# Optimization experiments

Hardware: AMD Instinct MI355X
Metric: run time of the kernel (lower is better)

Reference implementation:

```python
import jax, jax.numpy as jnp
import numpy as np

ATTRACTION_W = 1.0
REPULSION_W = 1.0
MARGIN = 0.3  # hardcoded local `margin = 0.3` in the torch forward


def setup_inputs() -> dict:
    key = jax.random.key(0)
    k1, k2, k3 = jax.random.split(key, 3)
    B, N, D, K = 16, 65536, 32, 512
    beta = jax.random.normal(k1, (B, N, 1), dtype=jnp.float32)
    embed = jax.random.normal(k2, (B, N, D), dtype=jnp.float32)
    # instance id per hit: -1 = background, 0..K-1 = instances
    sid = jax.random.randint(k3, (B, N), -1, K).astype(jnp.int32)
    # first K hits are the condensation points, one per instance
    sid = sid.at[:, :K].set(jnp.arange(K, dtype=jnp.int32)[None, :])
    is_cp = jnp.zeros((B, N), dtype=jnp.int32).at[:, :K].set(1)
    return {"beta": beta, "embed": embed, "slice_id": sid, "is_cp": is_cp, "num_instances": K}


def _per_batch(beta_b, emb_b, sid, iscp, K):
    # beta_b: [N], emb_b: [N, D], sid/iscp: [N]
    N = sid.shape[0]
    cp = iscp == 1
    valid = sid >= 0
    noncp = valid & ~cp  # non-cp signal hits
    pos = cp.sum().astype(jnp.float32)
    neg = jnp.float32(N) - pos  # noncp + background
    pos_w = jax.lax.stop_gradient(neg / (pos + 1e-6))
    w = jnp.where(cp, pos_w, jnp.where(noncp, 1.0, 2.0))
    # weighted BCE-with-logits, reduction='mean'
    x = beta_b
    y = cp.astype(jnp.float32)
    bce = jnp.maximum(x, 0.0) - x * y + jnp.log1p(jnp.exp(-jnp.abs(x)))
    beta_ce = (w * bce).mean()

    # segment id: valid hits -> sid, background -> dummy segment K (dropped)
    seg = jnp.where(valid, sid, K)
    counts = jax.ops.segment_sum(valid.astype(jnp.float32), seg, num_segments=K + 1)[:K]
    inst_exists = counts > 0  # the `unique()` set

    # first cp hit index per instance (sentinel N if instance has no cp)
    idxs = jnp.arange(N)
    first_cp = jax.ops.segment_min(jnp.where(cp & valid, idxs, N), seg, num_segments=K + 1)[:K]
    has_cp = first_cp < N
    safe_cp = jnp.minimum(first_cp, N - 1)
    cp_emb = emb_b[safe_cp]  # [K, D]
    cp_beta = beta_b[safe_cp]  # [K]

    # attraction: sum over instances (with a cp) of mean ||e_hit - e_cp||^2
    sid_c = jnp.clip(sid, 0, K - 1)
    d2 = ((emb_b - cp_emb[sid_c]) ** 2).sum(-1)  # [N]
    d2 = jnp.where(valid, d2, 0.0)
    seg_d2 = jax.ops.segment_sum(d2, seg, num_segments=K + 1)[:K]
    attr = (jnp.where(has_cp & inst_exists, seg_d2 / jnp.maximum(counts, 1.0), 0.0).sum()
            * ATTRACTION_W)

    # ranking: instances with exactly 1 cp and >0 noncp hits
    cp_count = jax.ops.segment_sum((cp & valid).astype(jnp.float32), seg, num_segments=K + 1)[:K]
    ncp_count = jax.ops.segment_sum(noncp.astype(jnp.float32), seg, num_segments=K + 1)[:K]
    r = jax.nn.relu(beta_b + MARGIN - cp_beta[sid_c])
    r = jnp.where(noncp, r, 0.0)
    seg_r = jax.ops.segment_sum(r, seg, num_segments=K + 1)[:K]
    qual = (cp_count == 1.0) & (ncp_count > 0)
    n_unique = inst_exists.sum().astype(jnp.float32)
    ranking = (jnp.where(qual, seg_r / jnp.maximum(ncp_count, 1.0), 0.0).sum()
               / jnp.maximum(n_unique, 1.0))

    beta_loss = beta_ce + 2.0 * ranking

    # repulsion over all cp hits; data has exactly one cp per instance so the
    # cp set equals cp_emb (K points), matching torch's emb_b[cp_idx]
    diff = cp_emb[:, None, :] - cp_emb[None, :, :]  # [K, K, D]
    rep = jnp.exp(-(diff ** 2).sum(-1)).mean() * REPULSION_W

    return beta_loss + attr + rep, beta_loss, attr, rep


def reference(beta, embed, slice_id, is_cp, num_instances):
    K = int(num_instances)
    beta2 = beta[..., 0]  # squeeze(-1)
    loss_b, bl, al, rl = jax.vmap(lambda b, e, s, c: _per_batch(b, e, s, c, K))(
        beta2, embed, slice_id, is_cp)
    return loss_b.mean(), bl.mean(), al.mean(), rl.mean()
```

## Files before the change

kernel.cpp:

```cpp
#include <hip/hip_runtime.h>
#include <math.h>

#define N_HITS 65536
#define K_INST 512
#define D_EMB  32
#define MARGIN 0.3f
#define BPB    64

__global__ void k_scan(const int* __restrict__ sid, const int* __restrict__ iscp,
                       int* first_cp, int* pos_cnt) {
    int b = blockIdx.y;
    int i = blockIdx.x * blockDim.x + threadIdx.x;
    int stride = gridDim.x * blockDim.x;
    for (; i < N_HITS; i += stride) {
        int c = iscp[b * N_HITS + i];
        if (c == 1) {
            atomicAdd(&pos_cnt[b], 1);
            int s = sid[b * N_HITS + i];
            if (s >= 0) atomicMin(&first_cp[b * K_INST + s], i);
        }
    }
}

__global__ void k_gather(const float* __restrict__ beta, const float4* __restrict__ embed4,
                         const int* __restrict__ first_cp,
                         float* cp_beta, float4* cp_emb4, int B) {
    int g = blockIdx.x * blockDim.x + threadIdx.x;
    int total = B * K_INST * 8;
    if (g >= total) return;
    int row = g >> 3, sub = g & 7;
    int b = row / K_INST;
    int fc = first_cp[row];
    int safe = min(fc, N_HITS - 1);
    cp_emb4[(size_t)row * 8 + sub] = embed4[((size_t)b * N_HITS + safe) * 8 + sub];
    if (sub == 0) cp_beta[row] = beta[b * N_HITS + safe];
}

__global__ __launch_bounds__(256) void k_main(
    const float*  __restrict__ beta,  const float4* __restrict__ embed4,
    const int*    __restrict__ sid_g, const int*    __restrict__ iscp_g,
    const float4* __restrict__ cp_emb4, const float* __restrict__ cp_beta,
    int* cnt_packed, float* seg_d2, float* seg_r,
    float* s_cp, float* s_ncp, float* s_bg) {
    __shared__ int   l_cnt[K_INST];
    __shared__ float l_d2[K_INST];
    __shared__ float l_r[K_INST];
    __shared__ float l_red[12];

    int b = blockIdx.y;
    int tid = threadIdx.x;
    for (int k = tid; k < K_INST; k += 256) { l_cnt[k] = 0; l_d2[k] = 0.f; l_r[k] = 0.f; }
    __syncthreads();

    int sub = tid & 7, hid = tid >> 3;
    const int hits = N_HITS / BPB;
    int base = blockIdx.x * hits;
    float a_cp = 0.f, a_ncp = 0.f, a_bg = 0.f;

    for (int it = 0; it < hits / 32; ++it) {
        int i = base + it * 32 + hid;
        int s = sid_g[b * N_HITS + i];
        int c = iscp_g[b * N_HITS + i];
        bool cp = (c == 1), valid = (s >= 0), noncp = valid && !cp;
        int sc = min(max(s, 0), K_INST - 1);

        float4 e  = embed4[((size_t)b * N_HITS + i) * 8 + sub];
        float4 ce = cp_emb4[((size_t)b * K_INST + sc) * 8 + sub];
        float dx = e.x - ce.x, dy = e.y - ce.y, dz = e.z - ce.z, dw = e.w - ce.w;
        float d2 = dx * dx + dy * dy + dz * dz + dw * dw;
        d2 += __shfl_xor(d2, 1);
        d2 += __shfl_xor(d2, 2);
        d2 += __shfl_xor(d2, 4);

        if (sub == 0) {
            float x = beta[b * N_HITS + i];
            float bce = fmaxf(x, 0.f) - (cp ? x : 0.f) + log1pf(__expf(-fabsf(x)));
            if (cp) a_cp += bce; else if (noncp) a_ncp += bce; else a_bg += bce;
            if (valid) {
                atomicAdd(&l_cnt[s], cp ? (1 << 20) : 1);
                atomicAdd(&l_d2[s], d2);
                if (noncp) {
                    float r = fmaxf(x + MARGIN - cp_beta[b * K_INST + s], 0.f);
                    atomicAdd(&l_r[s], r);
                }
            }
        }
    }

    for (int o = 32; o > 0; o >>= 1) {
        a_cp  += __shfl_down(a_cp, o);
        a_ncp += __shfl_down(a_ncp, o);
        a_bg  += __shfl_down(a_bg, o);
    }
    int wave = tid >> 6;
    if ((tid & 63) == 0) { l_red[wave] = a_cp; l_red[4 + wave] = a_ncp; l_red[8 + wave] = a_bg; }
    __syncthreads();
    if (tid == 0) {
        atomicAdd(&s_cp[b],  l_red[0] + l_red[1] + l_red[2]  + l_red[3]);
        atomicAdd(&s_ncp[b], l_red[4] + l_red[5] + l_red[6]  + l_red[7]);
        atomicAdd(&s_bg[b],  l_red[8] + l_red[9] + l_red[10] + l_red[11]);
    }
    for (int k = tid; k < K_INST; k += 256) {
        int   cv = l_cnt[k]; if (cv)        atomicAdd(&cnt_packed[b * K_INST + k], cv);
        float dv = l_d2[k];  if (dv != 0.f) atomicAdd(&seg_d2[b * K_INST + k], dv);
        float rv = l_r[k];   if (rv != 0.f) atomicAdd(&seg_r[b * K_INST + k], rv);
    }
}

__global__ __launch_bounds__(512) void k_seg(
    const int* __restrict__ cnt_packed, const float* __restrict__ seg_d2,
    const float* __restrict__ seg_r, const int* __restrict__ first_cp,
    float* attr_b, float* ranksum_b, float* nuniq_b) {
    __shared__ float red[3][8];
    int b = blockIdx.x, k = threadIdx.x;
    int v = cnt_packed[b * K_INST + k];
    int ncp = v & 0xFFFFF, cpc = v >> 20;
    int counts = ncp + cpc;
    int fc = first_cp[b * K_INST + k];
    bool has_cp = fc < N_HITS, exists = counts > 0;
    float attr = (has_cp && exists) ? seg_d2[b * K_INST + k] / fmaxf((float)counts, 1.f) : 0.f;
    float rank = (cpc == 1 && ncp > 0) ? seg_r[b * K_INST + k] / fmaxf((float)ncp, 1.f) : 0.f;
    float uq = exists ? 1.f : 0.f;
    for (int o = 32; o > 0; o >>= 1) {
        attr += __shfl_down(attr, o);
        rank += __shfl_down(rank, o);
        uq   += __shfl_down(uq, o);
    }
    int wave = k >> 6;
    if ((k & 63) == 0) { red[0][wave] = attr; red[1][wave] = rank; red[2][wave] = uq; }
    __syncthreads();
    if (k == 0) {
        float a = 0.f, r = 0.f, u = 0.f;
        for (int w = 0; w < 8; ++w) { a += red[0][w]; r += red[1][w]; u += red[2][w]; }
        attr_b[b] = a; ranksum_b[b] = r; nuniq_b[b] = u;
    }
}

__global__ __launch_bounds__(256) void k_rep(const float4* __restrict__ cp_emb4, float* rep_b) {
    __shared__ float4 tile[32 * 8];
    __shared__ float red[4];
    int b  = blockIdx.x >> 4;
    int t2 = blockIdx.x & 15;
    int tid = threadIdx.x;
    const float4* base = cp_emb4 + (size_t)b * K_INST * 8;

    float4 r0[8], r1[8];
#pragma unroll
    for (int c = 0; c < 8; ++c) {
        r0[c] = base[(size_t)(2 * tid) * 8 + c];
        r1[c] = base[(size_t)(2 * tid + 1) * 8 + c];
    }
    tile[tid] = base[(size_t)t2 * 256 + tid];
    __syncthreads();

    float acc = 0.f;
    for (int j = 0; j < 32; ++j) {
        float d2a = 0.f, d2b = 0.f;
#pragma unroll
        for (int c = 0; c < 8; ++c) {
            float4 e = tile[j * 8 + c];
            float ax = r0[c].x - e.x, ay = r0[c].y - e.y, az = r0[c].z - e.z, aw = r0[c].w - e.w;
            d2a += ax * ax + ay * ay + az * az + aw * aw;
            float bx = r1[c].x - e.x, by = r1[c].y - e.y, bz = r1[c].z - e.z, bw = r1[c].w - e.w;
            d2b += bx * bx + by * by + bz * bz + bw * bw;
        }
        acc += __expf(-d2a) + __expf(-d2b);
    }
    for (int o = 32; o > 0; o >>= 1) acc += __shfl_down(acc, o);
    int wave = tid >> 6;
    if ((tid & 63) == 0) red[wave] = acc;
    __syncthreads();
    if (tid == 0) atomicAdd(&rep_b[b], red[0] + red[1] + red[2] + red[3]);
}

__global__ void k_final(const int* __restrict__ pos_cnt,
                        const float* __restrict__ s_cp, const float* __restrict__ s_ncp,
                        const float* __restrict__ s_bg, const float* __restrict__ attr_b,
                        const float* __restrict__ ranksum_b, const float* __restrict__ nuniq_b,
                        const float* __restrict__ rep_b, float* out, int B) {
    int b = threadIdx.x;
    float loss = 0.f, bl = 0.f, at = 0.f, rp = 0.f;
    if (b < B) {
        float pos = (float)pos_cnt[b];
        float pw = ((float)N_HITS - pos) / (pos + 1e-6f);
        float bce = (pw * s_cp[b] + s_ncp[b] + 2.f * s_bg[b]) / (float)N_HITS;
        float rank = ranksum_b[b] / fmaxf(nuniq_b[b], 1.f);
        bl = bce + 2.f * rank;
        at = attr_b[b];
        rp = rep_b[b] / (float)(K_INST * K_INST);
        loss = bl + at + rp;
    }
    for (int o = 32; o > 0; o >>= 1) {
        loss += __shfl_down(loss, o);
        bl   += __shfl_down(bl, o);
        at   += __shfl_down(at, o);
        rp   += __shfl_down(rp, o);
    }
    if (b == 0) {
        float inv = 1.f / (float)B;
        out[0] = loss * inv;
        out[1] = bl * inv;
        out[2] = at * inv;
        out[3] = rp * inv;
    }
}

extern "C" void kernel_launch(void* const* d_in, const int* in_sizes, int n_in,
                              void* d_out, int out_size, void* d_ws, size_t ws_size,
                              hipStream_t stream) {
    const float*  beta   = (const float*)d_in[0];
    const float*  embed  = (const float*)d_in[1];
    const int*    sid    = (const int*)d_in[2];
    const int*    iscp   = (const int*)d_in[3];
    float* out = (float*)d_out;

    int BN = in_sizes[0];
    int B  = BN / N_HITS;
    int BK = B * K_INST;

    char* ws = (char*)d_ws;
    int*   cnt_packed = (int*)ws;
    float* seg_d2     = (float*)(ws + 4 * (size_t)BK);
    float* seg_r      = (float*)(ws + 8 * (size_t)BK);
    float* scal       = (float*)(ws + 12 * (size_t)BK);
    int*   pos_cnt  = (int*)scal;
    float* s_cp     = scal + 1 * B;
    float* s_ncp    = scal + 2 * B;
    float* s_bg     = scal + 3 * B;
    float* attr_b   = scal + 4 * B;
    float* rank_b   = scal + 5 * B;
    float* nuniq_b  = scal + 6 * B;
    float* rep_b    = scal + 7 * B;
    size_t zbytes = 12 * (size_t)BK + 32 * (size_t)B;
    int*    first_cp = (int*)(ws + zbytes);
    float*  cp_beta  = (float*)(ws + zbytes + 4 * (size_t)BK);
    float4* cp_emb4  = (float4*)(ws + zbytes + 8 * (size_t)BK);

    hipMemsetAsync(ws, 0, zbytes, stream);
    hipMemsetAsync(first_cp, 0x7F, 4 * (size_t)BK, stream);

    k_scan<<<dim3(16, B), 256, 0, stream>>>(sid, iscp, first_cp, pos_cnt);

    {
        int total = BK * 8;
        k_gather<<<(total + 255) / 256, 256, 0, stream>>>(beta, (const float4*)embed,
                                                          first_cp, cp_beta, cp_emb4, B);
    }

    k_main<<<dim3(BPB, B), 256, 0, stream>>>(beta, (const float4*)embed, sid, iscp,
                                             (const float4*)cp_emb4, cp_beta,
                                             cnt_packed, seg_d2, seg_r, s_cp, s_ncp, s_bg);

    k_seg<<<B, 512, 0, stream>>>(cnt_packed, seg_d2, seg_r, first_cp,
                                 attr_b, rank_b, nuniq_b);

    k_rep<<<B * 16, 256, 0, stream>>>((const float4*)cp_emb4, rep_b);

    k_final<<<1, 64, 0, stream>>>(pos_cnt, s_cp, s_ncp, s_bg, attr_b, rank_b,
                                  nuniq_b, rep_b, out, B);
}
```

Baseline: 296.3 us.

## Fuse scan+gather into per-batch prep kernel, merge tail kernels, prefetch main loop

```diff
diff --git a/kernel.cpp b/kernel.cpp
--- a/kernel.cpp
+++ b/kernel.cpp
@@ -3,37 +3,47 @@
 
 #define N_HITS 65536
 #define K_INST 512
-#define D_EMB  32
 #define MARGIN 0.3f
-#define BPB    64
-
-__global__ void k_scan(const int* __restrict__ sid, const int* __restrict__ iscp,
-                       int* first_cp, int* pos_cnt) {
-    int b = blockIdx.y;
-    int i = blockIdx.x * blockDim.x + threadIdx.x;
-    int stride = gridDim.x * blockDim.x;
-    for (; i < N_HITS; i += stride) {
-        int c = iscp[b * N_HITS + i];
+#define BPB    128
+
+__global__ __launch_bounds__(1024) void k_prep(
+    const float* __restrict__ beta, const float4* __restrict__ embed4,
+    const int* __restrict__ sid, const int* __restrict__ iscp,
+    int* first_cp_g, int* pos_cnt, float* cp_beta, float4* cp_emb4) {
+    __shared__ int lfc[K_INST];
+    __shared__ int lpos[16];
+    int b = blockIdx.x, tid = threadIdx.x;
+    for (int k = tid; k < K_INST; k += 1024) lfc[k] = N_HITS;
+    __syncthreads();
+
+    size_t bo = (size_t)b * N_HITS;
+    int pos = 0;
+    for (int i = tid; i < N_HITS; i += 1024) {
+        int c = iscp[bo + i];
         if (c == 1) {
-            atomicAdd(&pos_cnt[b], 1);
-            int s = sid[b * N_HITS + i];
-            if (s >= 0) atomicMin(&first_cp[b * K_INST + s], i);
-        }
-    }
-}
-
-__global__ void k_gather(const float* __restrict__ beta, const float4* __restrict__ embed4,
-                         const int* __restrict__ first_cp,
-                         float* cp_beta, float4* cp_emb4, int B) {
-    int g = blockIdx.x * blockDim.x + threadIdx.x;
-    int total = B * K_INST * 8;
-    if (g >= total) return;
-    int row = g >> 3, sub = g & 7;
-    int b = row / K_INST;
-    int fc = first_cp[row];
-    int safe = min(fc, N_HITS - 1);
-    cp_emb4[(size_t)row * 8 + sub] = embed4[((size_t)b * N_HITS + safe) * 8 + sub];
-    if (sub == 0) cp_beta[row] = beta[b * N_HITS + safe];
+            pos++;
+            int s = sid[bo + i];
+            if (s >= 0) atomicMin(&lfc[s], i);
+        }
+    }
+    for (int o = 32; o > 0; o >>= 1) pos += __shfl_down(pos, o);
+    if ((tid & 63) == 0) lpos[tid >> 6] = pos;
+    __syncthreads();
+    if (tid == 0) {
+        int t = 0;
+        for (int w = 0; w < 16; ++w) t += lpos[w];
+        pos_cnt[b] = t;
+    }
+    int sub = tid & 7;
+    for (int r = tid >> 3; r < K_INST; r += 128) {
+        int fc = lfc[r];
+        int safe = min(fc, N_HITS - 1);
+        cp_emb4[((size_t)b * K_INST + r) * 8 + sub] = embed4[(bo + safe) * 8 + sub];
+        if (sub == 0) {
+            cp_beta[b * K_INST + r] = beta[bo + safe];
+            first_cp_g[b * K_INST + r] = fc;
+        }
+    }
 }
 
 __global__ __launch_bounds__(256) void k_main(
@@ -47,24 +57,35 @@
     __shared__ float l_r[K_INST];
     __shared__ float l_red[12];
 
-    int b = blockIdx.y;
-    int tid = threadIdx.x;
+    int b = blockIdx.y, tid = threadIdx.x;
     for (int k = tid; k < K_INST; k += 256) { l_cnt[k] = 0; l_d2[k] = 0.f; l_r[k] = 0.f; }
     __syncthreads();
 
     int sub = tid & 7, hid = tid >> 3;
     const int hits = N_HITS / BPB;
+    const int iters = hits / 32;
+    size_t bo = (size_t)b * N_HITS;
     int base = blockIdx.x * hits;
     float a_cp = 0.f, a_ncp = 0.f, a_bg = 0.f;
 
-    for (int it = 0; it < hits / 32; ++it) {
-        int i = base + it * 32 + hid;
-        int s = sid_g[b * N_HITS + i];
-        int c = iscp_g[b * N_HITS + i];
+    int i = base + hid;
+    int s = sid_g[bo + i];
+    int c = iscp_g[bo + i];
+    float4 e = embed4[(bo + i) * 8 + sub];
+    float x = beta[bo + i];
+
+    for (int it = 0; it < iters; ++it) {
+        int inext = i + 32;
+        int s2 = 0, c2 = 0; float4 e2 = make_float4(0.f, 0.f, 0.f, 0.f); float x2 = 0.f;
+        if (it + 1 < iters) {
+            s2 = sid_g[bo + inext];
+            c2 = iscp_g[bo + inext];
+            e2 = embed4[(bo + inext) * 8 + sub];
+            x2 = beta[bo + inext];
+        }
+
         bool cp = (c == 1), valid = (s >= 0), noncp = valid && !cp;
         int sc = min(max(s, 0), K_INST - 1);
-
-        float4 e  = embed4[((size_t)b * N_HITS + i) * 8 + sub];
         float4 ce = cp_emb4[((size_t)b * K_INST + sc) * 8 + sub];
         float dx = e.x - ce.x, dy = e.y - ce.y, dz = e.z - ce.z, dw = e.w - ce.w;
         float d2 = dx * dx + dy * dy + dz * dz + dw * dw;
@@ -73,7 +94,6 @@
         d2 += __shfl_xor(d2, 4);
 
         if (sub == 0) {
-            float x = beta[b * N_HITS + i];
             float bce = fmaxf(x, 0.f) - (cp ? x : 0.f) + log1pf(__expf(-fabsf(x)));
             if (cp) a_cp += bce; else if (noncp) a_ncp += bce; else a_bg += bce;
             if (valid) {
@@ -85,6 +105,7 @@
                 }
             }
         }
+        i = inext; s = s2; c = c2; e = e2; x = x2;
     }
 
     for (int o = 32; o > 0; o >>= 1) {
@@ -107,101 +128,109 @@
     }
 }
 
-__global__ __launch_bounds__(512) void k_seg(
+__global__ __launch_bounds__(512) void k_tail(
+    const float4* __restrict__ cp_emb4,
     const int* __restrict__ cnt_packed, const float* __restrict__ seg_d2,
     const float* __restrict__ seg_r, const int* __restrict__ first_cp,
-    float* attr_b, float* ranksum_b, float* nuniq_b) {
-    __shared__ float red[3][8];
-    int b = blockIdx.x, k = threadIdx.x;
-    int v = cnt_packed[b * K_INST + k];
-    int ncp = v & 0xFFFFF, cpc = v >> 20;
-    int counts = ncp + cpc;
-    int fc = first_cp[b * K_INST + k];
-    bool has_cp = fc < N_HITS, exists = counts > 0;
-    float attr = (has_cp && exists) ? seg_d2[b * K_INST + k] / fmaxf((float)counts, 1.f) : 0.f;
-    float rank = (cpc == 1 && ncp > 0) ? seg_r[b * K_INST + k] / fmaxf((float)ncp, 1.f) : 0.f;
-    float uq = exists ? 1.f : 0.f;
-    for (int o = 32; o > 0; o >>= 1) {
-        attr += __shfl_down(attr, o);
-        rank += __shfl_down(rank, o);
-        uq   += __shfl_down(uq, o);
-    }
-    int wave = k >> 6;
-    if ((k & 63) == 0) { red[0][wave] = attr; red[1][wave] = rank; red[2][wave] = uq; }
-    __syncthreads();
-    if (k == 0) {
-        float a = 0.f, r = 0.f, u = 0.f;
-        for (int w = 0; w < 8; ++w) { a += red[0][w]; r += red[1][w]; u += red[2][w]; }
-        attr_b[b] = a; ranksum_b[b] = r; nuniq_b[b] = u;
-    }
-}
-
-__global__ __launch_bounds__(256) void k_rep(const float4* __restrict__ cp_emb4, float* rep_b) {
-    __shared__ float4 tile[32 * 8];
-    __shared__ float red[4];
-    int b  = blockIdx.x >> 4;
-    int t2 = blockIdx.x & 15;
+    const int* __restrict__ pos_cnt, const float* __restrict__ s_cp,
+    const float* __restrict__ s_ncp, const float* __restrict__ s_bg,
+    float* attr_b, float* rank_b, float* nuniq_b, float* rep_b,
+    int* ctr, float* out, int B) {
     int tid = threadIdx.x;
-    const float4* base = cp_emb4 + (size_t)b * K_INST * 8;
-
-    float4 r0[8], r1[8];
+    int nrep = B * 16;
+
+    if ((int)blockIdx.x < nrep) {
+        __shared__ float4 tile[32 * 8];
+        __shared__ float red[8];
+        int b = blockIdx.x >> 4, t2 = blockIdx.x & 15;
+        const float4* base = cp_emb4 + (size_t)b * K_INST * 8;
+        float4 r0[8];
 #pragma unroll
-    for (int c = 0; c < 8; ++c) {
-        r0[c] = base[(size_t)(2 * tid) * 8 + c];
-        r1[c] = base[(size_t)(2 * tid + 1) * 8 + c];
-    }
-    tile[tid] = base[(size_t)t2 * 256 + tid];
-    __syncthreads();
-
-    float acc = 0.f;
-    for (int j = 0; j < 32; ++j) {
-        float d2a = 0.f, d2b = 0.f;
+        for (int cc = 0; cc < 8; ++cc) r0[cc] = base[(size_t)tid * 8 + cc];
+        if (tid < 256) tile[tid] = base[(size_t)t2 * 256 + tid];
+        __syncthreads();
+        float acc = 0.f;
+        for (int j = 0; j < 32; ++j) {
+            float d2 = 0.f;
 #pragma unroll
-        for (int c = 0; c < 8; ++c) {
-            float4 e = tile[j * 8 + c];
-            float ax = r0[c].x - e.x, ay = r0[c].y - e.y, az = r0[c].z - e.z, aw = r0[c].w - e.w;
-            d2a += ax * ax + ay * ay + az * az + aw * aw;
-            float bx = r1[c].x - e.x, by = r1[c].y - e.y, bz = r1[c].z - e.z, bw = r1[c].w - e.w;
-            d2b += bx * bx + by * by + bz * bz + bw * bw;
-        }
-        acc += __expf(-d2a) + __expf(-d2b);
-    }
-    for (int o = 32; o > 0; o >>= 1) acc += __shfl_down(acc, o);
-    int wave = tid >> 6;
-    if ((tid & 63) == 0) red[wave] = acc;
-    __syncthreads();
-    if (tid == 0) atomicAdd(&rep_b[b], red[0] + red[1] + red[2] + red[3]);
-}
-
-__global__ void k_final(const int* __restrict__ pos_cnt,
-                        const float* __restrict__ s_cp, const float* __restrict__ s_ncp,
-                        const float* __restrict__ s_bg, const float* __restrict__ attr_b,
-                        const float* __restrict__ ranksum_b, const float* __restrict__ nuniq_b,
-                        const float* __restrict__ rep_b, float* out, int B) {
-    int b = threadIdx.x;
-    float loss = 0.f, bl = 0.f, at = 0.f, rp = 0.f;
-    if (b < B) {
-        float pos = (float)pos_cnt[b];
-        float pw = ((float)N_HITS - pos) / (pos + 1e-6f);
-        float bce = (pw * s_cp[b] + s_ncp[b] + 2.f * s_bg[b]) / (float)N_HITS;
-        float rank = ranksum_b[b] / fmaxf(nuniq_b[b], 1.f);
-        bl = bce + 2.f * rank;
-        at = attr_b[b];
-        rp = rep_b[b] / (float)(K_INST * K_INST);
-        loss = bl + at + rp;
-    }
-    for (int o = 32; o > 0; o >>= 1) {
-        loss += __shfl_down(loss, o);
-        bl   += __shfl_down(bl, o);
-        at   += __shfl_down(at, o);
-        rp   += __shfl_down(rp, o);
-    }
-    if (b == 0) {
-        float inv = 1.f / (float)B;
-        out[0] = loss * inv;
-        out[1] = bl * inv;
-        out[2] = at * inv;
-        out[3] = rp * inv;
+            for (int cc = 0; cc < 8; ++cc) {
+                float4 ev = tile[j * 8 + cc];
+                float ax = r0[cc].x - ev.x, ay = r0[cc].y - ev.y;
+                float az = r0[cc].z - ev.z, aw = r0[cc].w - ev.w;
+                d2 += ax * ax + ay * ay + az * az + aw * aw;
+            }
+            acc += __expf(-d2);
+        }
+        for (int o = 32; o > 0; o >>= 1) acc += __shfl_down(acc, o);
+        if ((tid & 63) == 0) red[tid >> 6] = acc;
+        __syncthreads();
+        if (tid == 0) {
+            float t = 0.f;
+            for (int w = 0; w < 8; ++w) t += red[w];
+            atomicAdd(&rep_b[b], t);
+        }
+    } else {
+        __shared__ float red2[3][8];
+        int b = blockIdx.x - nrep, k = tid;
+        int v = cnt_packed[b * K_INST + k];
+        int ncp = v & 0xFFFFF, cpc = v >> 20;
+        int counts = ncp + cpc;
+        int fc = first_cp[b * K_INST + k];
+        bool has_cp = fc < N_HITS, exists = counts > 0;
+        float attr = (has_cp && exists) ? seg_d2[b * K_INST + k] / fmaxf((float)counts, 1.f) : 0.f;
+        float rank = (cpc == 1 && ncp > 0) ? seg_r[b * K_INST + k] / fmaxf((float)ncp, 1.f) : 0.f;
+        float uq = exists ? 1.f : 0.f;
+        for (int o = 32; o > 0; o >>= 1) {
+            attr += __shfl_down(attr, o);
+            rank += __shfl_down(rank, o);
+            uq   += __shfl_down(uq, o);
+        }
+        if ((k & 63) == 0) { red2[0][k >> 6] = attr; red2[1][k >> 6] = rank; red2[2][k >> 6] = uq; }
+        __syncthreads();
+        if (k == 0) {
+            float a = 0.f, r = 0.f, u = 0.f;
+            for (int w = 0; w < 8; ++w) { a += red2[0][w]; r += red2[1][w]; u += red2[2][w]; }
+            attr_b[b] = a; rank_b[b] = r; nuniq_b[b] = u;
+        }
+    }
+
+    __shared__ int is_last;
+    __syncthreads();
+    if (tid == 0) {
+        __threadfence();
+        int v = atomicAdd(ctr, 1);
+        is_last = (v == (int)gridDim.x - 1);
+    }
+    __syncthreads();
+    if (is_last) {
+        __threadfence();
+        if (tid < 64) {
+            int b = tid;
+            float loss = 0.f, bl = 0.f, at = 0.f, rp = 0.f;
+            if (b < B) {
+                float pos = (float)pos_cnt[b];
+                float pw = ((float)N_HITS - pos) / (pos + 1e-6f);
+                float bce = (pw * s_cp[b] + s_ncp[b] + 2.f * s_bg[b]) / (float)N_HITS;
+                float rank = rank_b[b] / fmaxf(nuniq_b[b], 1.f);
+                bl = bce + 2.f * rank;
+                at = attr_b[b];
+                rp = rep_b[b] / (float)(K_INST * K_INST);
+                loss = bl + at + rp;
+            }
+            for (int o = 32; o > 0; o >>= 1) {
+                loss += __shfl_down(loss, o);
+                bl   += __shfl_down(bl, o);
+                at   += __shfl_down(at, o);
+                rp   += __shfl_down(rp, o);
+            }
+            if (tid == 0) {
+                float inv = 1.f / (float)B;
+                out[0] = loss * inv;
+                out[1] = bl * inv;
+                out[2] = at * inv;
+                out[3] = rp * inv;
+            }
+        }
     }
 }
 
@@ -231,31 +260,23 @@
     float* rank_b   = scal + 5 * B;
     float* nuniq_b  = scal + 6 * B;
     float* rep_b    = scal + 7 * B;
-    size_t zbytes = 12 * (size_t)BK + 32 * (size_t)B;
+    int*   ctr      = (int*)(scal + 8 * B);
+    size_t zbytes = 12 * (size_t)BK + 32 * (size_t)B + 16;
     int*    first_cp = (int*)(ws + zbytes);
     float*  cp_beta  = (float*)(ws + zbytes + 4 * (size_t)BK);
     float4* cp_emb4  = (float4*)(ws + zbytes + 8 * (size_t)BK);
 
     hipMemsetAsync(ws, 0, zbytes, stream);
-    hipMemsetAsync(first_cp, 0x7F, 4 * (size_t)BK, stream);
-
-    k_scan<<<dim3(16, B), 256, 0, stream>>>(sid, iscp, first_cp, pos_cnt);
-
-    {
-        int total = BK * 8;
-        k_gather<<<(total + 255) / 256, 256, 0, stream>>>(beta, (const float4*)embed,
-                                                          first_cp, cp_beta, cp_emb4, B);
-    }
+
+    k_prep<<<B, 1024, 0, stream>>>(beta, (const float4*)embed, sid, iscp,
+                                   first_cp, pos_cnt, cp_beta, cp_emb4);
 
     k_main<<<dim3(BPB, B), 256, 0, stream>>>(beta, (const float4*)embed, sid, iscp,
                                              (const float4*)cp_emb4, cp_beta,
                                              cnt_packed, seg_d2, seg_r, s_cp, s_ncp, s_bg);
 
-    k_seg<<<B, 512, 0, stream>>>(cnt_packed, seg_d2, seg_r, first_cp,
-                                 attr_b, rank_b, nuniq_b);
-
-    k_rep<<<B * 16, 256, 0, stream>>>((const float4*)cp_emb4, rep_b);
-
-    k_final<<<1, 64, 0, stream>>>(pos_cnt, s_cp, s_ncp, s_bg, attr_b, rank_b,
-                                  nuniq_b, rep_b, out, B);
-}
+    k_tail<<<B * 16 + B, 512, 0, stream>>>(cp_emb4, cnt_packed, seg_d2, seg_r,
+                                           first_cp, pos_cnt, s_cp, s_ncp, s_bg,
+                                           attr_b, rank_b, nuniq_b, rep_b,
+                                           ctr, out, B);
+}
```

Result: slower. 310.3 us (+4.7%).
